# Performance work log

Measured on AMD Instinct MI355X. Metric: run time of the kernel, lower is better.

## Reference

```python
import jax, jax.numpy as jnp
import numpy as np

N_NODES = 100000
N_EDGES = 1600000
HIDDEN = 128
LEAKY_SLOPE = 0.01  # torch F.leaky_relu default


def setup_inputs() -> dict:
    key = jax.random.key(0)
    k_x, k_wi, k_wj, k_h, k_t = jax.random.split(key, 5)
    x = jax.random.normal(k_x, (N_NODES, HIDDEN), dtype=jnp.float32)
    # nn.Linear(hidden, 1, bias=False) weights, stored as length-hidden vectors
    w_i = jax.random.normal(k_wi, (HIDDEN,), dtype=jnp.float32) * (1.0 / np.sqrt(HIDDEN))
    w_j = jax.random.normal(k_wj, (HIDDEN,), dtype=jnp.float32) * (1.0 / np.sqrt(HIDDEN))
    h = jax.random.randint(k_h, (N_EDGES,), 0, N_NODES, dtype=jnp.int32)
    t = jax.random.randint(k_t, (N_EDGES,), 0, N_NODES, dtype=jnp.int32)
    return {"x": x, "w_i": w_i, "w_j": w_j, "h": h, "t": t}


def reference(x, w_i, w_j, h, t):
    n = x.shape[0]
    # per-node attention scores, then gather onto edges
    s_i = x @ w_i  # [N]
    s_j = x @ w_j  # [N]
    e = s_i[h] + s_j[t]  # [E]
    e = jnp.where(e > 0, e, LEAKY_SLOPE * e).astype(jnp.float32)
    # segment softmax grouped by source node h (torch_geometric softmax(e, h))
    seg_max = jax.ops.segment_max(e, h, num_segments=n)  # [N], -inf for empty segments
    ex = jnp.exp(e - seg_max[h])
    seg_sum = jax.ops.segment_sum(ex, h, num_segments=n)  # [N]
    alpha = ex / seg_sum[h]  # [E]
    # spmm: out[r] = sum_{edges with h==r} alpha * x[t]
    out = jax.ops.segment_sum(alpha[:, None] * x[t], h, num_segments=n)  # [N, d]
    return jax.nn.relu(out)
```

## Files before the change

kernel.cpp:

```cpp
#include <hip/hip_runtime.h>
#include <string.h>

#define HIDDEN 128
#define LEAKY 0.01f
#define TILE 4096
#define BSH 6
#define BNODES 64
#define CAPB 2048

__device__ __forceinline__ unsigned int rne_bf16(float f) {
    unsigned int x = __float_as_uint(f);
    return (x + 0x7FFFu + ((x >> 16) & 1u)) >> 16;
}

template<bool CVT>
__global__ void scores_k(const float* __restrict__ x,
                         const float* __restrict__ w_i,
                         const float* __restrict__ w_j,
                         float* __restrict__ s_i,
                         float* __restrict__ s_j,
                         unsigned short* __restrict__ xb,
                         int n_nodes) {
    int w = blockIdx.x * 4 + (threadIdx.x >> 6);
    int lane = threadIdx.x & 63;
    int sub = lane & 31;
    int node = 2 * w + (lane >> 5);
    if (node >= n_nodes) return;
    const float4* xr = reinterpret_cast<const float4*>(x + (size_t)node * HIDDEN);
    float4 xv = xr[sub];
    if (CVT) {
        uint2 pk;
        pk.x = rne_bf16(xv.x) | (rne_bf16(xv.y) << 16);
        pk.y = rne_bf16(xv.z) | (rne_bf16(xv.w) << 16);
        reinterpret_cast<uint2*>(xb + (size_t)node * HIDDEN)[sub] = pk;
    }
    float4 wi = reinterpret_cast<const float4*>(w_i)[sub];
    float4 wj = reinterpret_cast<const float4*>(w_j)[sub];
    float di = xv.x * wi.x + xv.y * wi.y + xv.z * wi.z + xv.w * wi.w;
    float dj = xv.x * wj.x + xv.y * wj.y + xv.z * wj.z + xv.w * wj.w;
    #pragma unroll
    for (int off = 16; off > 0; off >>= 1) {
        di += __shfl_xor(di, off, 64);
        dj += __shfl_xor(dj, off, 64);
    }
    if (sub == 0) { s_i[node] = di; s_j[node] = dj; }
}

__global__ void histscatter_k(const float* __restrict__ s_i,
                              const float* __restrict__ s_j,
                              const int* __restrict__ h,
                              const int* __restrict__ t,
                              int* __restrict__ bucket_cur,
                              uint2* __restrict__ te,
                              int n_edges, int n_buckets) {
    extern __shared__ int smem[];
    int* lhist = smem;
    int* lbase = smem + n_buckets;
    int tid = threadIdx.x;
    for (int v = tid; v < n_buckets; v += 256) lhist[v] = 0;
    __syncthreads();
    int tbeg = blockIdx.x * TILE;
    int tend = min(tbeg + TILE, n_edges);
    #pragma unroll 1
    for (int s = 0; s < TILE / 1024; ++s) {
        int i0 = tbeg + s * 1024 + tid * 4;
        if (i0 + 4 <= tend) {
            int4 hv = *reinterpret_cast<const int4*>(h + i0);
            atomicAdd(&lhist[hv.x >> BSH], 1);
            atomicAdd(&lhist[hv.y >> BSH], 1);
            atomicAdd(&lhist[hv.z >> BSH], 1);
            atomicAdd(&lhist[hv.w >> BSH], 1);
        } else {
            for (int i = i0; i < tend; ++i) atomicAdd(&lhist[h[i] >> BSH], 1);
        }
    }
    __syncthreads();
    for (int v = tid; v < n_buckets; v += 256) {
        int c = lhist[v];
        lbase[v] = (c > 0) ? atomicAdd(&bucket_cur[v], c) : 0;
        lhist[v] = 0;
    }
    __syncthreads();
    #pragma unroll 1
    for (int s = 0; s < TILE / 1024; ++s) {
        int i0 = tbeg + s * 1024 + tid * 4;
        if (i0 + 4 <= tend) {
            int4 hv = *reinterpret_cast<const int4*>(h + i0);
            int4 tv = *reinterpret_cast<const int4*>(t + i0);
            int hh[4] = {hv.x, hv.y, hv.z, hv.w};
            int tt[4] = {tv.x, tv.y, tv.z, tv.w};
            float ex[4];
            #pragma unroll
            for (int k = 0; k < 4; ++k) {
                float e = s_i[hh[k]] + s_j[tt[k]];
                e = e > 0.0f ? e : LEAKY * e;
                ex[k] = __expf(e);
            }
            #pragma unroll
            for (int k = 0; k < 4; ++k) {
                int bkt = hh[k] >> BSH;
                int pin = lbase[bkt] + atomicAdd(&lhist[bkt], 1);
                if (pin < CAPB) {
                    uint2 en;
                    en.x = (unsigned)tt[k] |
                           ((unsigned)(hh[k] & (BNODES - 1)) << 17);
                    en.y = __float_as_uint(ex[k]);
                    te[(size_t)bkt * CAPB + pin] = en;
                }
            }
        } else {
            for (int i = i0; i < tend; ++i) {
                int hh = h[i], tt2 = t[i];
                float e = s_i[hh] + s_j[tt2];
                e = e > 0.0f ? e : LEAKY * e;
                float ex1 = __expf(e);
                int bkt = hh >> BSH;
                int pin = lbase[bkt] + atomicAdd(&lhist[bkt], 1);
                if (pin < CAPB) {
                    uint2 en;
                    en.x = (unsigned)tt2 |
                           ((unsigned)(hh & (BNODES - 1)) << 17);
                    en.y = __float_as_uint(ex1);
                    te[(size_t)bkt * CAPB + pin] = en;
                }
            }
        }
    }
}

__global__ void bucket_sort_k(uint2* __restrict__ te,
                              const int* __restrict__ bucket_cur,
                              int* __restrict__ node_beg,
                              int* __restrict__ node_cnt,
                              int n_nodes, int n_buckets) {
    __shared__ uint2 stage[CAPB];
    __shared__ int cnt[BNODES];
    __shared__ int off[BNODES];
    int tid = threadIdx.x;
    int bkt = blockIdx.x;
    size_t base = (size_t)bkt * CAPB;
    int deg_b = min(bucket_cur[bkt], CAPB);
    if (tid < BNODES) cnt[tid] = 0;
    __syncthreads();
    for (int i = tid; i < deg_b; i += 256) {
        uint2 en = te[base + i];
        stage[i] = en;
        atomicAdd(&cnt[en.x >> 17], 1);
    }
    __syncthreads();
    if (tid < BNODES) {
        int v = cnt[tid];
        int incl = v;
        #pragma unroll
        for (int o = 1; o < BNODES; o <<= 1) {
            int u = __shfl_up(incl, o, 64);
            if (tid >= o) incl += u;
        }
        int excl = incl - v;
        off[tid] = excl;
        int node = (bkt << BSH) + tid;
        if (node < n_nodes) {
            node_beg[node] = (int)base + excl;
            node_cnt[node] = v;
        }
        cnt[tid] = 0;
    }
    __syncthreads();
    for (int i = tid; i < deg_b; i += 256) {
        uint2 en = stage[i];
        int row = en.x >> 17;
        te[base + off[row] + atomicAdd(&cnt[row], 1)] = en;
    }
}

__global__ void aggregate_bf16_k(const unsigned short* __restrict__ xb,
                                 const int* __restrict__ node_beg,
                                 const int* __restrict__ node_cnt,
                                 const long long* __restrict__ te,
                                 float* __restrict__ out,
                                 int n_nodes) {
    int gtid = blockIdx.x * blockDim.x + threadIdx.x;
    int node = __builtin_amdgcn_readfirstlane(gtid >> 6);
    int lane = threadIdx.x & 63;
    if (node >= n_nodes) return;
    long long* dst = reinterpret_cast<long long*>(out + (size_t)node * HIDDEN) + lane;
    int beg = node_beg[node];
    int deg = node_cnt[node];
    if (deg <= 0) {
        __builtin_nontemporal_store(0LL, dst);
        return;
    }
    int end = beg + deg;
    float accx = 0.0f, accy = 0.0f, ssum = 0.0f;
    int j = beg;
    int main_end = beg + (deg & ~7);
    for (; j < main_end; j += 8) {
        long long tv[8];
        unsigned int u[8];
        #pragma unroll
        for (int k = 0; k < 8; ++k) tv[k] = te[j + k];
        #pragma unroll
        for (int k = 0; k < 8; ++k)
            u[k] = *reinterpret_cast<const unsigned int*>(
                xb + (size_t)((int)tv[k] & 0x1FFFF) * HIDDEN + 2 * lane);
        #pragma unroll
        for (int k = 0; k < 8; ++k) {
            float a = __int_as_float((int)(tv[k] >> 32));
            float fx = __uint_as_float(u[k] << 16);
            float fy = __uint_as_float(u[k] & 0xFFFF0000u);
            ssum += a;
            accx += a * fx;
            accy += a * fy;
        }
    }
    if (j < end) {
        long long tv[8];
        unsigned int u[8];
        #pragma unroll
        for (int k = 0; k < 8; ++k) {
            int jj = j + k;
            int jc = jj < end ? jj : end - 1;
            tv[k] = te[jc];
        }
        #pragma unroll
        for (int k = 0; k < 8; ++k)
            u[k] = *reinterpret_cast<const unsigned int*>(
                xb + (size_t)((int)tv[k] & 0x1FFFF) * HIDDEN + 2 * lane);
        #pragma unroll
        for (int k = 0; k < 8; ++k) {
            float a = __int_as_float((int)(tv[k] >> 32));
            a = (j + k < end) ? a : 0.0f;
            float fx = __uint_as_float(u[k] << 16);
            float fy = __uint_as_float(u[k] & 0xFFFF0000u);
            ssum += a;
            accx += a * fx;
            accy += a * fy;
        }
    }
    float inv = 1.0f / ssum;
    float ox = accx * inv, oy = accy * inv;
    float2 o;
    o.x = ox > 0.0f ? ox : 0.0f;
    o.y = oy > 0.0f ? oy : 0.0f;
    long long bits;
    memcpy(&bits, &o, 8);
    __builtin_nontemporal_store(bits, dst);
}

__global__ void aggregate_f32_k(const float* __restrict__ x,
                                const int* __restrict__ node_beg,
                                const int* __restrict__ node_cnt,
                                const uint2* __restrict__ te,
                                float* __restrict__ out,
                                int n_nodes) {
    int gtid = blockIdx.x * blockDim.x + threadIdx.x;
    int node = __builtin_amdgcn_readfirstlane(gtid >> 6);
    int lane = threadIdx.x & 63;
    if (node >= n_nodes) return;
    long long* dst = reinterpret_cast<long long*>(out + (size_t)node * HIDDEN) + lane;
    int beg = node_beg[node];
    int deg = node_cnt[node];
    if (deg <= 0) {
        __builtin_nontemporal_store(0LL, dst);
        return;
    }
    int end = beg + deg;
    float accx = 0.0f, accy = 0.0f, ssum = 0.0f;
    for (int j = beg; j < end; j += 8) {
        uint2 tv[8];
        float2 v[8];
        #pragma unroll
        for (int k = 0; k < 8; ++k) {
            int jj = j + k;
            int jc = jj < end ? jj : end - 1;
            tv[k] = te[jc];
        }
        #pragma unroll
        for (int k = 0; k < 8; ++k)
            v[k] = reinterpret_cast<const float2*>(
                x + (size_t)(tv[k].x & 0x1FFFF) * HIDDEN)[lane];
        #pragma unroll
        for (int k = 0; k < 8; ++k) {
            float a = __uint_as_float(tv[k].y);
            a = (j + k < end) ? a : 0.0f;
            ssum += a;
            accx += a * v[k].x;
            accy += a * v[k].y;
        }
    }
    float inv = 1.0f / ssum;
    float ox = accx * inv, oy = accy * inv;
    float2 o;
    o.x = ox > 0.0f ? ox : 0.0f;
    o.y = oy > 0.0f ? oy : 0.0f;
    long long bits;
    memcpy(&bits, &o, 8);
    __builtin_nontemporal_store(bits, dst);
}

extern "C" void kernel_launch(void* const* d_in, const int* in_sizes, int n_in,
                              void* d_out, int out_size, void* d_ws, size_t ws_size,
                              hipStream_t stream) {
    const float* x   = (const float*)d_in[0];
    const float* w_i = (const float*)d_in[1];
    const float* w_j = (const float*)d_in[2];
    const int*   h   = (const int*)d_in[3];
    const int*   t   = (const int*)d_in[4];
    float* out = (float*)d_out;

    const int n_nodes   = in_sizes[0] / HIDDEN;
    const int n_edges   = in_sizes[3];
    const int n_tiles   = (n_edges + TILE - 1) / TILE;
    const int n_buckets = (n_nodes + BNODES - 1) / BNODES;

    char* p = (char*)d_ws;
    float* s_i = (float*)p;        p += (size_t)n_nodes * 4;
    float* s_j = (float*)p;        p += (size_t)n_nodes * 4;
    int* node_beg = (int*)p;       p += (size_t)n_nodes * 4;
    int* node_cnt = (int*)p;       p += (size_t)n_nodes * 4;
    int* bucket_cur = (int*)p;     p += (size_t)n_buckets * 4;
    p = (char*)(((uintptr_t)p + 7) & ~(uintptr_t)7);
    uint2* te = (uint2*)p;         p += (size_t)n_buckets * CAPB * 8;
    unsigned short* xb = (unsigned short*)p;
    p += (size_t)n_nodes * HIDDEN * 2;
    const bool use_bf16 = ws_size >= (size_t)(p - (char*)d_ws);

    const int shmem2 = 2 * n_buckets * (int)sizeof(int);
    const int score_blocks = (((n_nodes + 1) / 2) + 3) / 4;

    hipMemsetAsync(bucket_cur, 0, (size_t)n_buckets * sizeof(int), stream);

    if (use_bf16)
        scores_k<true><<<score_blocks, 256, 0, stream>>>(
            x, w_i, w_j, s_i, s_j, xb, n_nodes);
    else
        scores_k<false><<<score_blocks, 256, 0, stream>>>(
            x, w_i, w_j, s_i, s_j, nullptr, n_nodes);

    histscatter_k<<<n_tiles, 256, shmem2, stream>>>(
        s_i, s_j, h, t, bucket_cur, te, n_edges, n_buckets);

    bucket_sort_k<<<n_buckets, 256, 0, stream>>>(
        te, bucket_cur, node_beg, node_cnt, n_nodes, n_buckets);

    {
        int blocks = (n_nodes * 64 + 255) / 256;
        if (use_bf16)
            aggregate_bf16_k<<<blocks, 256, 0, stream>>>(
                xb, node_beg, node_cnt,
                reinterpret_cast<const long long*>(te), out, n_nodes);
        else
            aggregate_f32_k<<<blocks, 256, 0, stream>>>(
                x, node_beg, node_cnt, te, out, n_nodes);
    }
}
```

Baseline: 153.9 us.

## Fuse per-tile histogram into scores kernel and drop the memset launch

Moves the per-tile bucket histogram pass out of the scatter kernel into the scores kernel, with histogram blocks and score blocks sharing one grid so the two independent passes run concurrently. Per-tile histograms are written to a global buffer that the scatter kernel reads back. Block 0 now zeroes bucket_cur, which replaces the hipMemsetAsync call. This adds an extra global histogram buffer (n_tiles*n_buckets ints) and its read/write traffic in exchange for overlapping the h read with the x read and removing one launch.

```diff
diff --git a/kernel.cpp b/kernel.cpp
--- a/kernel.cpp
+++ b/kernel.cpp
@@ -14,73 +14,90 @@
 }
 
 template<bool CVT>
-__global__ void scores_k(const float* __restrict__ x,
-                         const float* __restrict__ w_i,
-                         const float* __restrict__ w_j,
-                         float* __restrict__ s_i,
-                         float* __restrict__ s_j,
-                         unsigned short* __restrict__ xb,
-                         int n_nodes) {
-    int w = blockIdx.x * 4 + (threadIdx.x >> 6);
-    int lane = threadIdx.x & 63;
-    int sub = lane & 31;
-    int node = 2 * w + (lane >> 5);
-    if (node >= n_nodes) return;
-    const float4* xr = reinterpret_cast<const float4*>(x + (size_t)node * HIDDEN);
-    float4 xv = xr[sub];
-    if (CVT) {
-        uint2 pk;
-        pk.x = rne_bf16(xv.x) | (rne_bf16(xv.y) << 16);
-        pk.y = rne_bf16(xv.z) | (rne_bf16(xv.w) << 16);
-        reinterpret_cast<uint2*>(xb + (size_t)node * HIDDEN)[sub] = pk;
-    }
-    float4 wi = reinterpret_cast<const float4*>(w_i)[sub];
-    float4 wj = reinterpret_cast<const float4*>(w_j)[sub];
-    float di = xv.x * wi.x + xv.y * wi.y + xv.z * wi.z + xv.w * wi.w;
-    float dj = xv.x * wj.x + xv.y * wj.y + xv.z * wj.z + xv.w * wj.w;
-    #pragma unroll
-    for (int off = 16; off > 0; off >>= 1) {
-        di += __shfl_xor(di, off, 64);
-        dj += __shfl_xor(dj, off, 64);
-    }
-    if (sub == 0) { s_i[node] = di; s_j[node] = dj; }
-}
-
-__global__ void histscatter_k(const float* __restrict__ s_i,
-                              const float* __restrict__ s_j,
+__global__ void hist_scores_k(const float* __restrict__ x,
+                              const float* __restrict__ w_i,
+                              const float* __restrict__ w_j,
+                              float* __restrict__ s_i,
+                              float* __restrict__ s_j,
+                              unsigned short* __restrict__ xb,
                               const int* __restrict__ h,
-                              const int* __restrict__ t,
+                              int* __restrict__ hist_g,
                               int* __restrict__ bucket_cur,
-                              uint2* __restrict__ te,
-                              int n_edges, int n_buckets) {
+                              int n_nodes, int n_edges,
+                              int n_tiles, int n_buckets) {
+    extern __shared__ int lhist[];
+    int tid = threadIdx.x;
+    if ((int)blockIdx.x < n_tiles) {
+        if (blockIdx.x == 0)
+            for (int v = tid; v < n_buckets; v += 256) bucket_cur[v] = 0;
+        for (int v = tid; v < n_buckets; v += 256) lhist[v] = 0;
+        __syncthreads();
+        int tbeg = blockIdx.x * TILE;
+        int tend = min(tbeg + TILE, n_edges);
+        #pragma unroll 1
+        for (int s = 0; s < TILE / 1024; ++s) {
+            int i0 = tbeg + s * 1024 + tid * 4;
+            if (i0 + 4 <= tend) {
+                int4 hv = *reinterpret_cast<const int4*>(h + i0);
+                atomicAdd(&lhist[hv.x >> BSH], 1);
+                atomicAdd(&lhist[hv.y >> BSH], 1);
+                atomicAdd(&lhist[hv.z >> BSH], 1);
+                atomicAdd(&lhist[hv.w >> BSH], 1);
+            } else {
+                for (int i = i0; i < tend; ++i) atomicAdd(&lhist[h[i] >> BSH], 1);
+            }
+        }
+        __syncthreads();
+        int* dst = hist_g + (size_t)blockIdx.x * n_buckets;
+        for (int v = tid; v < n_buckets; v += 256) dst[v] = lhist[v];
+    } else {
+        int w = (blockIdx.x - n_tiles) * 4 + (tid >> 6);
+        int lane = tid & 63;
+        int sub = lane & 31;
+        int node = 2 * w + (lane >> 5);
+        if (node >= n_nodes) return;
+        const float4* xr = reinterpret_cast<const float4*>(x + (size_t)node * HIDDEN);
+        float4 xv = xr[sub];
+        if (CVT) {
+            uint2 pk;
+            pk.x = rne_bf16(xv.x) | (rne_bf16(xv.y) << 16);
+            pk.y = rne_bf16(xv.z) | (rne_bf16(xv.w) << 16);
+            reinterpret_cast<uint2*>(xb + (size_t)node * HIDDEN)[sub] = pk;
+        }
+        float4 wi = reinterpret_cast<const float4*>(w_i)[sub];
+        float4 wj = reinterpret_cast<const float4*>(w_j)[sub];
+        float di = xv.x * wi.x + xv.y * wi.y + xv.z * wi.z + xv.w * wi.w;
+        float dj = xv.x * wj.x + xv.y * wj.y + xv.z * wj.z + xv.w * wj.w;
+        #pragma unroll
+        for (int off = 16; off > 0; off >>= 1) {
+            di += __shfl_xor(di, off, 64);
+            dj += __shfl_xor(dj, off, 64);
+        }
+        if (sub == 0) { s_i[node] = di; s_j[node] = dj; }
+    }
+}
+
+__global__ void binscatter_k(const float* __restrict__ s_i,
+                             const float* __restrict__ s_j,
+                             const int* __restrict__ h,
+                             const int* __restrict__ t,
+                             const int* __restrict__ hist_g,
+                             int* __restrict__ bucket_cur,
+                             uint2* __restrict__ te,
+                             int n_edges, int n_buckets) {
     extern __shared__ int smem[];
-    int* lhist = smem;
-    int* lbase = smem + n_buckets;
+    int* lbase = smem;
+    int* lcur  = smem + n_buckets;
     int tid = threadIdx.x;
-    for (int v = tid; v < n_buckets; v += 256) lhist[v] = 0;
+    const int* src = hist_g + (size_t)blockIdx.x * n_buckets;
+    for (int v = tid; v < n_buckets; v += 256) {
+        int c = src[v];
+        lbase[v] = (c > 0) ? atomicAdd(&bucket_cur[v], c) : 0;
+        lcur[v] = 0;
+    }
     __syncthreads();
     int tbeg = blockIdx.x * TILE;
     int tend = min(tbeg + TILE, n_edges);
-    #pragma unroll 1
-    for (int s = 0; s < TILE / 1024; ++s) {
-        int i0 = tbeg + s * 1024 + tid * 4;
-        if (i0 + 4 <= tend) {
-            int4 hv = *reinterpret_cast<const int4*>(h + i0);
-            atomicAdd(&lhist[hv.x >> BSH], 1);
-            atomicAdd(&lhist[hv.y >> BSH], 1);
-            atomicAdd(&lhist[hv.z >> BSH], 1);
-            atomicAdd(&lhist[hv.w >> BSH], 1);
-        } else {
-            for (int i = i0; i < tend; ++i) atomicAdd(&lhist[h[i] >> BSH], 1);
-        }
-    }
-    __syncthreads();
-    for (int v = tid; v < n_buckets; v += 256) {
-        int c = lhist[v];
-        lbase[v] = (c > 0) ? atomicAdd(&bucket_cur[v], c) : 0;
-        lhist[v] = 0;
-    }
-    __syncthreads();
     #pragma unroll 1
     for (int s = 0; s < TILE / 1024; ++s) {
         int i0 = tbeg + s * 1024 + tid * 4;
@@ -99,7 +116,7 @@
             #pragma unroll
             for (int k = 0; k < 4; ++k) {
                 int bkt = hh[k] >> BSH;
-                int pin = lbase[bkt] + atomicAdd(&lhist[bkt], 1);
+                int pin = lbase[bkt] + atomicAdd(&lcur[bkt], 1);
                 if (pin < CAPB) {
                     uint2 en;
                     en.x = (unsigned)tt[k] |
@@ -115,7 +132,7 @@
                 e = e > 0.0f ? e : LEAKY * e;
                 float ex1 = __expf(e);
                 int bkt = hh >> BSH;
-                int pin = lbase[bkt] + atomicAdd(&lhist[bkt], 1);
+                int pin = lbase[bkt] + atomicAdd(&lcur[bkt], 1);
                 if (pin < CAPB) {
                     uint2 en;
                     en.x = (unsigned)tt2 |
@@ -319,26 +336,28 @@
     int* node_beg = (int*)p;       p += (size_t)n_nodes * 4;
     int* node_cnt = (int*)p;       p += (size_t)n_nodes * 4;
     int* bucket_cur = (int*)p;     p += (size_t)n_buckets * 4;
+    int* hist_g = (int*)p;         p += (size_t)n_tiles * n_buckets * 4;
     p = (char*)(((uintptr_t)p + 7) & ~(uintptr_t)7);
     uint2* te = (uint2*)p;         p += (size_t)n_buckets * CAPB * 8;
     unsigned short* xb = (unsigned short*)p;
     p += (size_t)n_nodes * HIDDEN * 2;
     const bool use_bf16 = ws_size >= (size_t)(p - (char*)d_ws);
 
+    const int shmem1 = n_buckets * (int)sizeof(int);
     const int shmem2 = 2 * n_buckets * (int)sizeof(int);
     const int score_blocks = (((n_nodes + 1) / 2) + 3) / 4;
 
-    hipMemsetAsync(bucket_cur, 0, (size_t)n_buckets * sizeof(int), stream);
-
     if (use_bf16)
-        scores_k<true><<<score_blocks, 256, 0, stream>>>(
-            x, w_i, w_j, s_i, s_j, xb, n_nodes);
+        hist_scores_k<true><<<n_tiles + score_blocks, 256, shmem1, stream>>>(
+            x, w_i, w_j, s_i, s_j, xb, h, hist_g, bucket_cur,
+            n_nodes, n_edges, n_tiles, n_buckets);
     else
-        scores_k<false><<<score_blocks, 256, 0, stream>>>(
-            x, w_i, w_j, s_i, s_j, nullptr, n_nodes);
-
-    histscatter_k<<<n_tiles, 256, shmem2, stream>>>(
-        s_i, s_j, h, t, bucket_cur, te, n_edges, n_buckets);
+        hist_scores_k<false><<<n_tiles + score_blocks, 256, shmem1, stream>>>(
+            x, w_i, w_j, s_i, s_j, nullptr, h, hist_g, bucket_cur,
+            n_nodes, n_edges, n_tiles, n_buckets);
+
+    binscatter_k<<<n_tiles, 256, shmem2, stream>>>(
+        s_i, s_j, h, t, hist_g, bucket_cur, te, n_edges, n_buckets);
 
     bucket_sort_k<<<n_buckets, 256, 0, stream>>>(
         te, bucket_cur, node_beg, node_cnt, n_nodes, n_buckets);
```

Result: faster. 148.7 us (median of 2 runs) (-3.4%).
